# Performance work log

Measured on AMD Instinct MI355X. Metric: run time of the kernel, lower is better.

Reference implementation:

```python
import jax, jax.numpy as jnp
import numpy as np

P = 2  # sampling ratio: keep top ceil(M/p) measurements


def setup_inputs() -> dict:
    key = jax.random.key(0)
    k1, k2, k3 = jax.random.split(key, 3)
    B, H, W, C = 8, 1024, 1024, 3
    Y = jax.random.normal(k1, (B, H, W, C), dtype=jnp.float32)
    # build()-time Z0 components: abs ~ N(0.5, 0.1), angle ~ N(0, 0.5*sqrt(pi))
    Z0_abs = 0.5 + 0.1 * jax.random.normal(k2, (1, 1, H, W), dtype=jnp.float32)
    Z0_angle = (0.5 * np.pi ** 0.5) * jax.random.normal(k3, (1, 1, H, W), dtype=jnp.float32)
    return {"Y": Y, "Z0_abs": Z0_abs, "Z0_angle": Z0_angle}


def _make_Z0(Z0_abs, Z0_angle):
    # Z0 = |Z0| * exp(i*angle), Frobenius-normalized over spatial axes (2,3)
    Z0 = Z0_abs.astype(jnp.complex64) * jnp.exp(1j * Z0_angle.astype(jnp.complex64))
    fro = jnp.sqrt(jnp.sum(jnp.abs(Z0) ** 2, axis=(2, 3), keepdims=True)).astype(jnp.complex64)
    return Z0 / fro


def reference(Y, Z0_abs, Z0_angle):
    B, H, W, C = Y.shape
    M = H * W * C
    R = int(np.ceil(M / P))
    # transpose NHWC -> NCHW, scale by original S[2] (= W)
    Y_S = jnp.transpose(Y.astype(jnp.float32), (0, 3, 1, 2)) / jnp.float32(W)
    y_s = Y_S.reshape(B, M)
    # threshold = R-th largest value per batch (== descending-sorted index R-1)
    thr = jax.lax.top_k(y_s, R)[0][:, -1]  # [B]
    Ytr = (Y_S >= thr[:, None, None, None]).astype(jnp.float32)  # [B,C,H,W]
    Z0 = _make_Z0(Z0_abs, Z0_angle)
    return Ytr, Z0
```

## Files before the change

### kernel.cpp

```cpp
#include <hip/hip_runtime.h>
#include <math.h>

#define BATCH 8
#define HH 1024
#define WW 1024
#define CC 3
#define MTOT (HH*WW*CC)
#define RSEL 1572864u
#define NSEG 96
#define SEGCAP 3072u

#define U_HI 0xBC800000u
#define U_LO 0x437FFFFFu

#define WS_SCNT_OFF   0u
#define WS_CHI_OFF    4096u
#define WS_NPART_OFF  8192u
#define WS_THR_OFF    12288u
#define WS_NORM_OFF   12352u
#define WS_BUF_OFF    16384u

__device__ __forceinline__ unsigned int fmap(float x) {
    unsigned int b = __float_as_uint(x);
    return (b & 0x80000000u) ? ~b : (b | 0x80000000u);
}

__global__ void pass1_kernel(const float* __restrict__ Y,
                             const float* __restrict__ zabs,
                             unsigned int* __restrict__ buf,
                             unsigned int* __restrict__ scnt,
                             unsigned int* __restrict__ chi,
                             float* __restrict__ npart) {
    const int tid = threadIdx.x;
    const int bx = blockIdx.x;

    if (blockIdx.y == 8) {
        float s = 0.f;
        const int n4z = HH * WW / 4;
        for (int i = bx * blockDim.x + tid; i < n4z; i += NSEG * blockDim.x) {
            float4 v = ((const float4*)zabs)[i];
            s += v.x * v.x + v.y * v.y + v.z * v.z + v.w * v.w;
        }
        for (int d = 32; d > 0; d >>= 1) s += __shfl_down(s, d);
        __shared__ float ls[4];
        if ((tid & 63) == 0) ls[tid >> 6] = s;
        __syncthreads();
        if (tid == 0) npart[bx] = ls[0] + ls[1] + ls[2] + ls[3];
        return;
    }

    __shared__ unsigned int lbuf[2048];
    __shared__ unsigned int lcnt;
    __shared__ unsigned int red[4];
    const int b = blockIdx.y;
    if (tid == 0) lcnt = 0u;
    __syncthreads();

    const float4* Y4 = (const float4*)(Y + (size_t)b * MTOT);
    unsigned int* seg = buf + (size_t)(b * NSEG + bx) * SEGCAP;
    const int n4 = MTOT / 4;
    const int stride = NSEG * blockDim.x;
    const int iters = n4 / stride;
    unsigned int hcnt = 0u;
    unsigned int base = 0u;

    for (int it = 0; it < iters; it++) {
        int i = it * stride + bx * blockDim.x + tid;
        float4 v = Y4[i];
        unsigned int u;
#define PROC(comp) u = fmap(comp); \
        if (u >= U_HI) hcnt++; \
        else if (u >= U_LO) { unsigned int p = atomicAdd(&lcnt, 1u); if (p < 2048u) lbuf[p] = u; }
        PROC(v.x) PROC(v.y) PROC(v.z) PROC(v.w)
#undef PROC
        __syncthreads();
        unsigned int n = lcnt;
        if (n >= 1024u) {
            for (unsigned int j = tid; j < n; j += blockDim.x) {
                unsigned int p = base + j;
                if (p < SEGCAP) seg[p] = lbuf[j];
            }
            base += n;
            __syncthreads();
            if (tid == 0) lcnt = 0u;
        }
        __syncthreads();
    }
    unsigned int n = lcnt;
    if (n > 2048u) n = 2048u;
    for (unsigned int j = tid; j < n; j += blockDim.x) {
        unsigned int p = base + j;
        if (p < SEGCAP) seg[p] = lbuf[j];
    }
    base += lcnt;
    if (tid == 0) scnt[b * NSEG + bx] = base;

    for (int d = 32; d > 0; d >>= 1) hcnt += __shfl_down(hcnt, d);
    if ((tid & 63) == 0) red[tid >> 6] = hcnt;
    __syncthreads();
    if (tid == 0) chi[b * NSEG + bx] = red[0] + red[1] + red[2] + red[3];
}

__global__ void __launch_bounds__(1024) refine_kernel(
        const float* __restrict__ Y,
        const unsigned int* __restrict__ buf,
        const unsigned int* __restrict__ scnt,
        const unsigned int* __restrict__ chi,
        const float* __restrict__ npart,
        unsigned int* __restrict__ thr,
        float* __restrict__ normsum) {
    const int tid = threadIdx.x;

    if (blockIdx.x == 8) {
        if (tid == 0) {
            float s = 0.f;
            for (int i = 0; i < NSEG; i++) s += npart[i];
            *normsum = s;
        }
        return;
    }

    __shared__ unsigned int hist[4096];
    __shared__ unsigned int segcnt[NSEG];
    __shared__ unsigned int waveSums[16];
    __shared__ unsigned int selBin, selBase;
    __shared__ unsigned int mode_s, target_s;
    const int b = blockIdx.x;
    const int lane = tid & 63, wid = tid >> 6;

    if (tid < NSEG) {
        unsigned int c = scnt[b * NSEG + tid];
        segcnt[tid] = (c > SEGCAP) ? SEGCAP : c;
    }
    if (tid == 0) {
        unsigned int tot = 0u, Ch = 0u, mx = 0u;
        for (int j = 0; j < NSEG; j++) {
            unsigned int c = scnt[b * NSEG + j];
            if (c > mx) mx = c;
            tot += c;
            Ch += chi[b * NSEG + j];
        }
        int fb = (mx > SEGCAP) || (Ch >= RSEL) || (Ch + tot < RSEL);
        mode_s = (unsigned int)fb;
        target_s = fb ? RSEL : (RSEL - Ch);
    }
    __syncthreads();
    const int fb = (int)mode_s;
    unsigned int target = target_s;
    const unsigned int* bseg = buf + (size_t)b * NSEG * SEGCAP;
    const float* Yb = Y + (size_t)b * MTOT;

    unsigned int d1 = 0, d2 = 0;

    for (int level = 0; level < 3; level++) {
        const int nb  = (level < 2) ? 4096 : 256;
        const int bpt = (level < 2) ? 4 : 1;
        for (int i = tid; i < nb; i += 1024) hist[i] = 0u;
        if (tid == 0) { selBin = 0u; selBase = 0u; }
        __syncthreads();

#define HISTO(u) do { \
            if (level == 0) atomicAdd(&hist[(u) >> 20], 1u); \
            else if (level == 1) { if (((u) >> 20) == d1) atomicAdd(&hist[((u) >> 8) & 0xFFFu], 1u); } \
            else { if (((u) >> 8) == ((d1 << 12) | d2)) atomicAdd(&hist[(u) & 0xFFu], 1u); } \
        } while (0)

        if (fb) {
            for (unsigned int i = tid; i < (unsigned int)MTOT; i += 1024u) {
                unsigned int u = fmap(Yb[i]);
                HISTO(u);
            }
        } else {
            for (int sj = wid; sj < NSEG; sj += 16) {
                const unsigned int cj = segcnt[sj];
                const unsigned int* sp = bseg + (size_t)sj * SEGCAP;
                for (unsigned int k = lane; k < cj; k += 64u) {
                    unsigned int u = sp[k];
                    HISTO(u);
                }
            }
        }
#undef HISTO
        __syncthreads();
        unsigned int c[4] = {0u, 0u, 0u, 0u};
        unsigned int s = 0u;
        const int nthr = nb / bpt;
        if (tid < nthr)
            for (int k = 0; k < bpt; k++) { c[k] = hist[nb - 1 - (tid * bpt + k)]; s += c[k]; }
        unsigned int incl = s;
        for (int d = 1; d < 64; d <<= 1) {
            unsigned int v = __shfl_up(incl, d);
            if (lane >= d) incl += v;
        }
        if (lane == 63) waveSums[wid] = incl;
        __syncthreads();
        if (tid < 16) {
            unsigned int w = waveSums[tid];
            for (int d = 1; d < 16; d <<= 1) {
                unsigned int v = __shfl_up(w, d);
                if (tid >= d) w += v;
            }
            waveSums[tid] = w;
        }
        __syncthreads();
        incl += (wid > 0) ? waveSums[wid - 1] : 0u;
        unsigned int excl = incl - s;
        if (s > 0u && excl < target && incl >= target) {
            unsigned int run = excl;
            for (int k = 0; k < bpt; k++) {
                if (run + c[k] >= target) {
                    selBin = (unsigned int)(nb - 1 - (tid * bpt + k));
                    selBase = run;
                    break;
                }
                run += c[k];
            }
        }
        __syncthreads();
        if (level == 0) d1 = selBin;
        else if (level == 1) d2 = selBin;
        target -= selBase;
        __syncthreads();
    }
    if (tid == 0) thr[b] = (d1 << 20) | (d2 << 8) | selBin;
}

__global__ void thresh_z_kernel(const float* __restrict__ Y,
                                const unsigned int* __restrict__ thr,
                                const float* __restrict__ zabs,
                                const float* __restrict__ zang,
                                const float* __restrict__ normsum,
                                float* __restrict__ out,
                                float* __restrict__ outz, int interleaved) {
    if (blockIdx.x < 8192) {
        int p = blockIdx.x * blockDim.x + threadIdx.x;
        int w4 = p & 255;
        int h  = (p >> 8) & 1023;
        int b  = p >> 18;
        unsigned int tu = thr[b];
        const float4* src = (const float4*)(Y + ((size_t)((b * HH + h) * WW) + (size_t)w4 * 4) * CC);
        float4 a0 = src[0], a1 = src[1], a2 = src[2];
        float4 r0, r1, r2;
        r0.x = (fmap(a0.x) >= tu) ? 1.f : 0.f;
        r0.y = (fmap(a0.w) >= tu) ? 1.f : 0.f;
        r0.z = (fmap(a1.z) >= tu) ? 1.f : 0.f;
        r0.w = (fmap(a2.y) >= tu) ? 1.f : 0.f;
        r1.x = (fmap(a0.y) >= tu) ? 1.f : 0.f;
        r1.y = (fmap(a1.x) >= tu) ? 1.f : 0.f;
        r1.z = (fmap(a1.w) >= tu) ? 1.f : 0.f;
        r1.w = (fmap(a2.z) >= tu) ? 1.f : 0.f;
        r2.x = (fmap(a0.z) >= tu) ? 1.f : 0.f;
        r2.y = (fmap(a1.y) >= tu) ? 1.f : 0.f;
        r2.z = (fmap(a2.x) >= tu) ? 1.f : 0.f;
        r2.w = (fmap(a2.w) >= tu) ? 1.f : 0.f;
        size_t base = ((size_t)(b * CC) * HH + h) * WW;
        ((float4*)(out + base))[w4]                        = r0;
        ((float4*)(out + base + (size_t)HH * WW))[w4]      = r1;
        ((float4*)(out + base + (size_t)2 * HH * WW))[w4]  = r2;
    } else {
        int i = (blockIdx.x - 8192) * blockDim.x + threadIdx.x;
        float inv = 1.0f / sqrtf(*normsum);
        float2 a = ((const float2*)zabs)[i];
        float2 g = ((const float2*)zang)[i];
        float s0, c0, s1, c1;
        __sincosf(g.x, &s0, &c0);
        __sincosf(g.y, &s1, &c1);
        if (interleaved) {
            float4 o;
            o.x = a.x * c0 * inv; o.y = a.x * s0 * inv;
            o.z = a.y * c1 * inv; o.w = a.y * s1 * inv;
            ((float4*)outz)[i] = o;
        } else {
            float2 o;
            o.x = a.x * c0 * inv; o.y = a.y * c1 * inv;
            ((float2*)outz)[i] = o;
        }
    }
}

extern "C" void kernel_launch(void* const* d_in, const int* in_sizes, int n_in,
                              void* d_out, int out_size, void* d_ws, size_t ws_size,
                              hipStream_t stream) {
    const float* Y    = (const float*)d_in[0];
    const float* zabs = (const float*)d_in[1];
    const float* zang = (const float*)d_in[2];
    float* out = (float*)d_out;

    unsigned char* ws = (unsigned char*)d_ws;
    unsigned int* scnt  = (unsigned int*)(ws + WS_SCNT_OFF);
    unsigned int* chi   = (unsigned int*)(ws + WS_CHI_OFF);
    float*        npart = (float*)(ws + WS_NPART_OFF);
    unsigned int* thr   = (unsigned int*)(ws + WS_THR_OFF);
    float*        norm  = (float*)(ws + WS_NORM_OFF);
    unsigned int* buf   = (unsigned int*)(ws + WS_BUF_OFF);

    dim3 g1(NSEG, 9);
    pass1_kernel<<<g1, 256, 0, stream>>>(Y, zabs, buf, scnt, chi, npart);
    refine_kernel<<<9, 1024, 0, stream>>>(Y, buf, scnt, chi, npart, thr, norm);

    size_t zoff = (size_t)BATCH * CC * HH * WW;
    int zfloats = out_size - (int)zoff;
    int interleaved = (zfloats >= 2 * HH * WW) ? 1 : 0;
    thresh_z_kernel<<<8192 + 2048, 256, 0, stream>>>(
        Y, thr, zabs, zang, norm, out, out + zoff, interleaved);
}
```

Baseline: 244.8 us.

## Fuse provisional threshold output into candidate pass and fix up only ambiguous elements

The first pass now writes a provisional mask while it reads Y: elements above the high bound become 1 and all others 0. It also records (position, key) pairs for candidates that fall inside the ambiguous band into per-block segments. The final kernel then only rewrites those candidate positions once the exact threshold is known, so Y is no longer re-read in full, unless a fallback flag forces the full recompute. This removes one full read of Y at the cost of scattered writes for candidates and a larger 8-byte candidate buffer. The refine kernel's count reduction is also parallelised across 1024 threads.

```diff
diff --git a/kernel.cpp b/kernel.cpp
--- a/kernel.cpp
+++ b/kernel.cpp
@@ -5,20 +5,23 @@
 #define HH 1024
 #define WW 1024
 #define CC 3
-#define MTOT (HH*WW*CC)
+#define HW (HH*WW)
+#define CHW (CC*HH*WW)
 #define RSEL 1572864u
-#define NSEG 96
-#define SEGCAP 3072u
+#define NSEG 1024
+#define SEGCAP 512u
+#define NZB 96
 
 #define U_HI 0xBC800000u
 #define U_LO 0x437FFFFFu
 
 #define WS_SCNT_OFF   0u
-#define WS_CHI_OFF    4096u
-#define WS_NPART_OFF  8192u
-#define WS_THR_OFF    12288u
-#define WS_NORM_OFF   12352u
-#define WS_BUF_OFF    16384u
+#define WS_CHI_OFF    32768u
+#define WS_NPART_OFF  65536u
+#define WS_THR_OFF    66048u
+#define WS_FB_OFF     66112u
+#define WS_NORM_OFF   66176u
+#define WS_BUF_OFF    131072u
 
 __device__ __forceinline__ unsigned int fmap(float x) {
     unsigned int b = __float_as_uint(x);
@@ -27,17 +30,19 @@
 
 __global__ void pass1_kernel(const float* __restrict__ Y,
                              const float* __restrict__ zabs,
-                             unsigned int* __restrict__ buf,
+                             float* __restrict__ out,
+                             uint2* __restrict__ buf,
                              unsigned int* __restrict__ scnt,
                              unsigned int* __restrict__ chi,
                              float* __restrict__ npart) {
     const int tid = threadIdx.x;
-    const int bx = blockIdx.x;
-
-    if (blockIdx.y == 8) {
+    const int blk = blockIdx.x;
+
+    if (blk >= 8192) {
+        int zb = blk - 8192;
         float s = 0.f;
-        const int n4z = HH * WW / 4;
-        for (int i = bx * blockDim.x + tid; i < n4z; i += NSEG * blockDim.x) {
+        const int n4z = HW / 4;
+        for (int i = zb * blockDim.x + tid; i < n4z; i += NZB * blockDim.x) {
             float4 v = ((const float4*)zabs)[i];
             s += v.x * v.x + v.y * v.y + v.z * v.z + v.w * v.w;
         }
@@ -45,76 +50,72 @@
         __shared__ float ls[4];
         if ((tid & 63) == 0) ls[tid >> 6] = s;
         __syncthreads();
-        if (tid == 0) npart[bx] = ls[0] + ls[1] + ls[2] + ls[3];
+        if (tid == 0) npart[zb] = ls[0] + ls[1] + ls[2] + ls[3];
         return;
     }
 
-    __shared__ unsigned int lbuf[2048];
+    __shared__ uint2 lbuf[SEGCAP];
     __shared__ unsigned int lcnt;
     __shared__ unsigned int red[4];
-    const int b = blockIdx.y;
     if (tid == 0) lcnt = 0u;
     __syncthreads();
 
-    const float4* Y4 = (const float4*)(Y + (size_t)b * MTOT);
-    unsigned int* seg = buf + (size_t)(b * NSEG + bx) * SEGCAP;
-    const int n4 = MTOT / 4;
-    const int stride = NSEG * blockDim.x;
-    const int iters = n4 / stride;
+    int p  = blk * 256 + tid;
+    int w4 = p & 255;
+    int h  = (p >> 8) & 1023;
+    int b  = p >> 18;
+    const float4* src = (const float4*)(Y + ((size_t)((b * HH + h) * WW) + (size_t)w4 * 4) * CC);
+    float4 a0 = src[0], a1 = src[1], a2 = src[2];
     unsigned int hcnt = 0u;
-    unsigned int base = 0u;
-
-    for (int it = 0; it < iters; it++) {
-        int i = it * stride + bx * blockDim.x + tid;
-        float4 v = Y4[i];
-        unsigned int u;
-#define PROC(comp) u = fmap(comp); \
-        if (u >= U_HI) hcnt++; \
-        else if (u >= U_LO) { unsigned int p = atomicAdd(&lcnt, 1u); if (p < 2048u) lbuf[p] = u; }
-        PROC(v.x) PROC(v.y) PROC(v.z) PROC(v.w)
+    const unsigned int posbase = (unsigned int)(h * WW + w4 * 4);
+
+    float4 r0, r1, r2;
+#define PROC(val, c, px, dst) do { \
+        unsigned int u = fmap(val); \
+        if (u >= U_HI) { dst = 1.f; hcnt++; } \
+        else { dst = 0.f; \
+            if (u >= U_LO) { \
+                unsigned int q = atomicAdd(&lcnt, 1u); \
+                if (q < SEGCAP) lbuf[q] = make_uint2((unsigned)(c) * HW + posbase + (px), u); \
+            } } \
+    } while (0)
+    PROC(a0.x, 0, 0, r0.x); PROC(a0.w, 0, 1, r0.y); PROC(a1.z, 0, 2, r0.z); PROC(a2.y, 0, 3, r0.w);
+    PROC(a0.y, 1, 0, r1.x); PROC(a1.x, 1, 1, r1.y); PROC(a1.w, 1, 2, r1.z); PROC(a2.z, 1, 3, r1.w);
+    PROC(a0.z, 2, 0, r2.x); PROC(a1.y, 2, 1, r2.y); PROC(a2.x, 2, 2, r2.z); PROC(a2.w, 2, 3, r2.w);
 #undef PROC
-        __syncthreads();
-        unsigned int n = lcnt;
-        if (n >= 1024u) {
-            for (unsigned int j = tid; j < n; j += blockDim.x) {
-                unsigned int p = base + j;
-                if (p < SEGCAP) seg[p] = lbuf[j];
-            }
-            base += n;
-            __syncthreads();
-            if (tid == 0) lcnt = 0u;
-        }
-        __syncthreads();
-    }
+    size_t base = ((size_t)(b * CC) * HH + h) * WW;
+    ((float4*)(out + base))[w4]                       = r0;
+    ((float4*)(out + base + (size_t)HW))[w4]          = r1;
+    ((float4*)(out + base + (size_t)2 * HW))[w4]      = r2;
+
+    __syncthreads();
     unsigned int n = lcnt;
-    if (n > 2048u) n = 2048u;
-    for (unsigned int j = tid; j < n; j += blockDim.x) {
-        unsigned int p = base + j;
-        if (p < SEGCAP) seg[p] = lbuf[j];
-    }
-    base += lcnt;
-    if (tid == 0) scnt[b * NSEG + bx] = base;
+    unsigned int nw = (n > SEGCAP) ? SEGCAP : n;
+    uint2* seg = buf + (size_t)blk * SEGCAP;
+    for (unsigned int j = tid; j < nw; j += blockDim.x) seg[j] = lbuf[j];
+    if (tid == 0) scnt[blk] = n;
 
     for (int d = 32; d > 0; d >>= 1) hcnt += __shfl_down(hcnt, d);
     if ((tid & 63) == 0) red[tid >> 6] = hcnt;
     __syncthreads();
-    if (tid == 0) chi[b * NSEG + bx] = red[0] + red[1] + red[2] + red[3];
+    if (tid == 0) chi[blk] = red[0] + red[1] + red[2] + red[3];
 }
 
 __global__ void __launch_bounds__(1024) refine_kernel(
         const float* __restrict__ Y,
-        const unsigned int* __restrict__ buf,
+        const uint2* __restrict__ buf,
         const unsigned int* __restrict__ scnt,
         const unsigned int* __restrict__ chi,
         const float* __restrict__ npart,
         unsigned int* __restrict__ thr,
+        unsigned int* __restrict__ fbflag,
         float* __restrict__ normsum) {
     const int tid = threadIdx.x;
 
     if (blockIdx.x == 8) {
         if (tid == 0) {
             float s = 0.f;
-            for (int i = 0; i < NSEG; i++) s += npart[i];
+            for (int i = 0; i < NZB; i++) s += npart[i];
             *normsum = s;
         }
         return;
@@ -123,32 +124,40 @@
     __shared__ unsigned int hist[4096];
     __shared__ unsigned int segcnt[NSEG];
     __shared__ unsigned int waveSums[16];
+    __shared__ unsigned int stats[16][3];
     __shared__ unsigned int selBin, selBase;
     __shared__ unsigned int mode_s, target_s;
     const int b = blockIdx.x;
     const int lane = tid & 63, wid = tid >> 6;
 
-    if (tid < NSEG) {
-        unsigned int c = scnt[b * NSEG + tid];
-        segcnt[tid] = (c > SEGCAP) ? SEGCAP : c;
-    }
+    unsigned int sc = scnt[b * NSEG + tid];
+    unsigned int ch = chi[b * NSEG + tid];
+    segcnt[tid] = (sc > SEGCAP) ? SEGCAP : sc;
+    unsigned int t_tot = sc, t_ch = ch, t_mx = sc;
+    for (int d = 32; d > 0; d >>= 1) {
+        t_tot += __shfl_down(t_tot, d);
+        t_ch  += __shfl_down(t_ch, d);
+        unsigned int m = __shfl_down(t_mx, d);
+        if (m > t_mx) t_mx = m;
+    }
+    if (lane == 0) { stats[wid][0] = t_tot; stats[wid][1] = t_ch; stats[wid][2] = t_mx; }
+    __syncthreads();
     if (tid == 0) {
         unsigned int tot = 0u, Ch = 0u, mx = 0u;
-        for (int j = 0; j < NSEG; j++) {
-            unsigned int c = scnt[b * NSEG + j];
-            if (c > mx) mx = c;
-            tot += c;
-            Ch += chi[b * NSEG + j];
+        for (int j = 0; j < 16; j++) {
+            tot += stats[j][0]; Ch += stats[j][1];
+            if (stats[j][2] > mx) mx = stats[j][2];
         }
         int fb = (mx > SEGCAP) || (Ch >= RSEL) || (Ch + tot < RSEL);
         mode_s = (unsigned int)fb;
         target_s = fb ? RSEL : (RSEL - Ch);
+        fbflag[b] = (unsigned int)fb;
     }
     __syncthreads();
     const int fb = (int)mode_s;
     unsigned int target = target_s;
-    const unsigned int* bseg = buf + (size_t)b * NSEG * SEGCAP;
-    const float* Yb = Y + (size_t)b * MTOT;
+    const uint2* bseg = buf + (size_t)b * NSEG * SEGCAP;
+    const float* Yb = Y + (size_t)b * CHW;
 
     unsigned int d1 = 0, d2 = 0;
 
@@ -166,16 +175,16 @@
         } while (0)
 
         if (fb) {
-            for (unsigned int i = tid; i < (unsigned int)MTOT; i += 1024u) {
+            for (unsigned int i = tid; i < (unsigned int)CHW; i += 1024u) {
                 unsigned int u = fmap(Yb[i]);
                 HISTO(u);
             }
         } else {
             for (int sj = wid; sj < NSEG; sj += 16) {
                 const unsigned int cj = segcnt[sj];
-                const unsigned int* sp = bseg + (size_t)sj * SEGCAP;
+                const uint2* sp = bseg + (size_t)sj * SEGCAP;
                 for (unsigned int k = lane; k < cj; k += 64u) {
-                    unsigned int u = sp[k];
+                    unsigned int u = sp[k].y;
                     HISTO(u);
                 }
             }
@@ -225,40 +234,55 @@
     if (tid == 0) thr[b] = (d1 << 20) | (d2 << 8) | selBin;
 }
 
-__global__ void thresh_z_kernel(const float* __restrict__ Y,
-                                const unsigned int* __restrict__ thr,
-                                const float* __restrict__ zabs,
-                                const float* __restrict__ zang,
-                                const float* __restrict__ normsum,
-                                float* __restrict__ out,
-                                float* __restrict__ outz, int interleaved) {
+__global__ void fixup_z_kernel(const float* __restrict__ Y,
+                               const uint2* __restrict__ buf,
+                               const unsigned int* __restrict__ scnt,
+                               const unsigned int* __restrict__ thr,
+                               const unsigned int* __restrict__ fbflag,
+                               const float* __restrict__ zabs,
+                               const float* __restrict__ zang,
+                               const float* __restrict__ normsum,
+                               float* __restrict__ out,
+                               float* __restrict__ outz, int interleaved) {
+    const int tid = threadIdx.x;
     if (blockIdx.x < 8192) {
-        int p = blockIdx.x * blockDim.x + threadIdx.x;
-        int w4 = p & 255;
-        int h  = (p >> 8) & 1023;
-        int b  = p >> 18;
+        const int blk = blockIdx.x;
+        const int b = blk >> 10;
         unsigned int tu = thr[b];
-        const float4* src = (const float4*)(Y + ((size_t)((b * HH + h) * WW) + (size_t)w4 * 4) * CC);
-        float4 a0 = src[0], a1 = src[1], a2 = src[2];
-        float4 r0, r1, r2;
-        r0.x = (fmap(a0.x) >= tu) ? 1.f : 0.f;
-        r0.y = (fmap(a0.w) >= tu) ? 1.f : 0.f;
-        r0.z = (fmap(a1.z) >= tu) ? 1.f : 0.f;
-        r0.w = (fmap(a2.y) >= tu) ? 1.f : 0.f;
-        r1.x = (fmap(a0.y) >= tu) ? 1.f : 0.f;
-        r1.y = (fmap(a1.x) >= tu) ? 1.f : 0.f;
-        r1.z = (fmap(a1.w) >= tu) ? 1.f : 0.f;
-        r1.w = (fmap(a2.z) >= tu) ? 1.f : 0.f;
-        r2.x = (fmap(a0.z) >= tu) ? 1.f : 0.f;
-        r2.y = (fmap(a1.y) >= tu) ? 1.f : 0.f;
-        r2.z = (fmap(a2.x) >= tu) ? 1.f : 0.f;
-        r2.w = (fmap(a2.w) >= tu) ? 1.f : 0.f;
-        size_t base = ((size_t)(b * CC) * HH + h) * WW;
-        ((float4*)(out + base))[w4]                        = r0;
-        ((float4*)(out + base + (size_t)HH * WW))[w4]      = r1;
-        ((float4*)(out + base + (size_t)2 * HH * WW))[w4]  = r2;
+        if (fbflag[b] == 0u) {
+            unsigned int n = scnt[blk];
+            const uint2* seg = buf + (size_t)blk * SEGCAP;
+            float* ob = out + (size_t)b * CHW;
+            for (unsigned int j = tid; j < n; j += 256u) {
+                uint2 e = seg[j];
+                ob[e.x] = (e.y >= tu) ? 1.f : 0.f;
+            }
+        } else {
+            int p  = blk * 256 + tid;
+            int w4 = p & 255;
+            int h  = (p >> 8) & 1023;
+            const float4* src = (const float4*)(Y + ((size_t)((b * HH + h) * WW) + (size_t)w4 * 4) * CC);
+            float4 a0 = src[0], a1 = src[1], a2 = src[2];
+            float4 r0, r1, r2;
+            r0.x = (fmap(a0.x) >= tu) ? 1.f : 0.f;
+            r0.y = (fmap(a0.w) >= tu) ? 1.f : 0.f;
+            r0.z = (fmap(a1.z) >= tu) ? 1.f : 0.f;
+            r0.w = (fmap(a2.y) >= tu) ? 1.f : 0.f;
+            r1.x = (fmap(a0.y) >= tu) ? 1.f : 0.f;
+            r1.y = (fmap(a1.x) >= tu) ? 1.f : 0.f;
+            r1.z = (fmap(a1.w) >= tu) ? 1.f : 0.f;
+            r1.w = (fmap(a2.z) >= tu) ? 1.f : 0.f;
+            r2.x = (fmap(a0.z) >= tu) ? 1.f : 0.f;
+            r2.y = (fmap(a1.y) >= tu) ? 1.f : 0.f;
+            r2.z = (fmap(a2.x) >= tu) ? 1.f : 0.f;
+            r2.w = (fmap(a2.w) >= tu) ? 1.f : 0.f;
+            size_t base = ((size_t)(b * CC) * HH + h) * WW;
+            ((float4*)(out + base))[w4]                   = r0;
+            ((float4*)(out + base + (size_t)HW))[w4]      = r1;
+            ((float4*)(out + base + (size_t)2 * HW))[w4]  = r2;
+        }
     } else {
-        int i = (blockIdx.x - 8192) * blockDim.x + threadIdx.x;
+        int i = (blockIdx.x - 8192) * blockDim.x + tid;
         float inv = 1.0f / sqrtf(*normsum);
         float2 a = ((const float2*)zabs)[i];
         float2 g = ((const float2*)zang)[i];
@@ -291,16 +315,16 @@
     unsigned int* chi   = (unsigned int*)(ws + WS_CHI_OFF);
     float*        npart = (float*)(ws + WS_NPART_OFF);
     unsigned int* thr   = (unsigned int*)(ws + WS_THR_OFF);
+    unsigned int* fbf   = (unsigned int*)(ws + WS_FB_OFF);
     float*        norm  = (float*)(ws + WS_NORM_OFF);
-    unsigned int* buf   = (unsigned int*)(ws + WS_BUF_OFF);
-
-    dim3 g1(NSEG, 9);
-    pass1_kernel<<<g1, 256, 0, stream>>>(Y, zabs, buf, scnt, chi, npart);
-    refine_kernel<<<9, 1024, 0, stream>>>(Y, buf, scnt, chi, npart, thr, norm);
-
-    size_t zoff = (size_t)BATCH * CC * HH * WW;
+    uint2*        buf   = (uint2*)(ws + WS_BUF_OFF);
+
+    pass1_kernel<<<8192 + NZB, 256, 0, stream>>>(Y, zabs, out, buf, scnt, chi, npart);
+    refine_kernel<<<9, 1024, 0, stream>>>(Y, buf, scnt, chi, npart, thr, fbf, norm);
+
+    size_t zoff = (size_t)BATCH * CHW;
     int zfloats = out_size - (int)zoff;
-    int interleaved = (zfloats >= 2 * HH * WW) ? 1 : 0;
-    thresh_z_kernel<<<8192 + 2048, 256, 0, stream>>>(
-        Y, thr, zabs, zang, norm, out, out + zoff, interleaved);
-}
+    int interleaved = (zfloats >= 2 * HW) ? 1 : 0;
+    fixup_z_kernel<<<8192 + 2048, 256, 0, stream>>>(
+        Y, buf, scnt, thr, fbf, zabs, zang, norm, out, out + zoff, interleaved);
+}
```

New measurement: 285.2 us. +16.5%, slower.
